# Performance work log

Measured on AMD Instinct MI355X. Metric: run time of the kernel, lower is better.

The kernel has to match this reference:

```python
import jax, jax.numpy as jnp
import numpy as np


def setup_inputs() -> dict:
    key = jax.random.key(0)
    k1, k2, k3, k4, k5 = jax.random.split(key, 5)
    B, L, D = 8, 4096, 64
    return {
        "Q": jax.random.normal(k1, (B, L, D), dtype=jnp.float32),
        "K": jax.random.normal(k2, (B, L, D), dtype=jnp.float32),
        "V": jax.random.normal(k3, (B, L, D), dtype=jnp.float32),
        "sent_embed_slice": jax.random.normal(k4, (B, D), dtype=jnp.float32),
        "proj": jax.random.normal(k5, (D, D), dtype=jnp.float32),  # fixed phi projection (M, d)
        "qkv_size": 64,
        "masked": 1,
    }


def _phi(X, proj, M):
    # X: (B, L, d). Original applies phi per timestep slice x = X[:, t, :] of shape (B, d)
    # phi(x) = (1/sqrt(M)) * exp(-0.5 * ||x||_F) * exp(proj @ x), Frobenius norm over the (B, d) slice.
    logits = jnp.einsum("bld,md->blm", X, proj)            # (B, L, M)
    scale = jnp.exp(-0.5 * jnp.sqrt(jnp.sum(X * X, axis=(0, 2))))  # per-timestep scalar, (L,)
    return jnp.exp(logits) * scale[None, :, None] / jnp.sqrt(jnp.asarray(M, jnp.float32))


def reference(Q, K, V, sent_embed_slice, proj, qkv_size, masked):
    M = qkv_size
    phi_q = _phi(Q, proj, M)  # (B, L, M)
    phi_k = _phi(K, proj, M)  # (B, L, M)
    if masked:
        # causal running sums: KV_t = sum_{j<=t} phi_k_j outer V_j ; N_t = sum_{j<=t} phi_k_j
        KV = jnp.cumsum(phi_k[:, :, :, None] * V[:, :, None, :], axis=1)  # (B, L, M, D)
        Nc = jnp.cumsum(phi_k, axis=1)                                    # (B, L, M)
        num = jnp.einsum("blm,blmd->bld", phi_q, KV)
        r = jnp.einsum("blm,blm->bl", phi_q, Nc)
        return num / (r + jnp.sign(r) * 1e-6)[:, :, None]
    else:
        KV = jnp.einsum("blm,bld->bmd", phi_k, V)     # (B, M, D)
        Ns = jnp.sum(phi_k, axis=1)                    # (B, M); broadcast over D like torch norm_sum
        num = jnp.einsum("blm,bmd->bld", phi_q, KV)
        r = jnp.einsum("blm,bm->bl", phi_q, Ns)
        return num / r[:, :, None]
```

## Files before the change

kernel.cpp:

```cpp
#include <hip/hip_runtime.h>
#include <math.h>

#define BB 8
#define LL 4096
#define DD 64
#define SS 64
#define NCHUNK 64
#define STATE 4160

typedef __attribute__((ext_vector_type(8))) short s16x8;
typedef __attribute__((ext_vector_type(8))) unsigned short u16x8;
typedef __attribute__((ext_vector_type(4))) float f32x4;

#define MFMA(a, b, c) __builtin_amdgcn_mfma_f32_16x16x32_bf16((a), (b), (c), 0, 0, 0)

static __device__ __forceinline__ unsigned short f2bf(float x) {
  unsigned int u = __builtin_bit_cast(unsigned int, x);
  u += 0x7FFFu + ((u >> 16) & 1u);
  return (unsigned short)(u >> 16);
}
static __device__ __forceinline__ float bf2f(unsigned short h) {
  unsigned int u = ((unsigned int)h) << 16;
  return __builtin_bit_cast(float, u);
}

static __device__ __forceinline__ s16x8 ld_frag(const unsigned short* base, int row0, int ks) {
  const int lane = threadIdx.x & 63;
  const int r = row0 + (lane & 15);
  const int idx = r * 64 + ((ks * 32 + ((lane & 48) >> 1)) ^ ((r & 7) << 3));
  return *(const s16x8*)(base + idx);
}

static __device__ __forceinline__ void stage_hl(unsigned short* __restrict__ Sh,
                                                unsigned short* __restrict__ Sl,
                                                const float* __restrict__ src, int tid) {
#pragma unroll
  for (int it = 0; it < 2; ++it) {
    const int g = tid + it * 256;
    const int row = g >> 3;
    const int c0 = (g & 7) * 8;
    const float4 x0 = *(const float4*)(src + row * 64 + c0);
    const float4 x1 = *(const float4*)(src + row * 64 + c0 + 4);
    const float xs[8] = {x0.x, x0.y, x0.z, x0.w, x1.x, x1.y, x1.z, x1.w};
    u16x8 h, l;
#pragma unroll
    for (int k = 0; k < 8; ++k) {
      const unsigned short hh = f2bf(xs[k]);
      h[k] = hh;
      l[k] = f2bf(xs[k] - bf2f(hh));
    }
    const int idx = row * 64 + (c0 ^ ((row & 7) << 3));
    *(u16x8*)(Sh + idx) = h;
    *(u16x8*)(Sl + idx) = l;
  }
}

static __device__ __forceinline__ void logits3(const unsigned short* Ah_, const unsigned short* Al_,
                                               const unsigned short* Bh_, const unsigned short* Bl_,
                                               int w, f32x4 acc[4]) {
  s16x8 ah[2], al[2];
#pragma unroll
  for (int ks = 0; ks < 2; ++ks) {
    ah[ks] = ld_frag(Ah_, w * 16, ks);
    al[ks] = ld_frag(Al_, w * 16, ks);
  }
#pragma unroll
  for (int ct = 0; ct < 4; ++ct) {
#pragma unroll
    for (int ks = 0; ks < 2; ++ks) {
      const s16x8 bh = ld_frag(Bh_, ct * 16, ks);
      const s16x8 bl = ld_frag(Bl_, ct * 16, ks);
      acc[ct] = MFMA(ah[ks], bh, acc[ct]);
      acc[ct] = MFMA(ah[ks], bl, acc[ct]);
      acc[ct] = MFMA(al[ks], bh, acc[ct]);
    }
  }
}

static __device__ __forceinline__ void phi_store_row(unsigned short* dst, const f32x4* acc,
                                                     const float* sc, int w) {
  const int lane = threadIdx.x & 63;
#pragma unroll
  for (int ri = 0; ri < 4; ++ri) {
    const int t = w * 16 + ((lane & 48) >> 2) + ri;
#pragma unroll
    for (int ct = 0; ct < 4; ++ct) {
      const int m = ct * 16 + (lane & 15);
      dst[t * 64 + (m ^ ((t & 7) << 3))] = f2bf(__expf(acc[ct][ri]) * sc[ri]);
    }
  }
}

static __device__ __forceinline__ void phi_store_col(unsigned short* dst, const f32x4* acc,
                                                     const float* sc, int w) {
  const int lane = threadIdx.x & 63;
#pragma unroll
  for (int ri = 0; ri < 4; ++ri) {
    const int t = w * 16 + ((lane & 48) >> 2) + ri;
#pragma unroll
    for (int ct = 0; ct < 4; ++ct) {
      const int m = ct * 16 + (lane & 15);
      dst[m * 64 + (t ^ ((m & 7) << 3))] = f2bf(__expf(acc[ct][ri]) * sc[ri]);
    }
  }
}

static __device__ __forceinline__ void stage_vhalf(float* __restrict__ F, const float* __restrict__ src,
                                                   int tid) {
#pragma unroll
  for (int it = 0; it < 2; ++it) {
    const int g = tid + it * 256;
    const int row = g >> 4;
    const int col = (g & 15) * 4;
    *(float4*)(F + row * 64 + col) = *(const float4*)(src + row * 64 + col);
  }
}

static __device__ __forceinline__ void vtrans_half(unsigned short* __restrict__ Gh,
                                                   unsigned short* __restrict__ Hl,
                                                   const float* __restrict__ F, int tid, int half) {
  const int d = tid & 63;
  const int tb = (tid >> 6) * 8;
  float v[8];
#pragma unroll
  for (int k = 0; k < 8; ++k) v[k] = F[(tb + k) * 64 + d];
  u16x8 hh, ll;
#pragma unroll
  for (int k = 0; k < 8; ++k) {
    const unsigned short h = f2bf(v[k]);
    hh[k] = h;
    ll[k] = f2bf(v[k] - bf2f(h));
  }
  const int idx = d * 64 + ((half * 32 + tb) ^ ((d & 7) << 3));
  *(u16x8*)(Gh + idx) = hh;
  *(u16x8*)(Hl + idx) = ll;
}

__global__ __launch_bounds__(256) void k_scales(const float* __restrict__ Q,
                                                const float* __restrict__ K,
                                                float* __restrict__ ws) {
  const int t = blockIdx.x * 4 + (threadIdx.x >> 6);
  const int lane = threadIdx.x & 63;
  const int b = lane >> 3;
  const int d0 = (lane & 7) * 8;
  const size_t base = (size_t)b * (LL * DD) + (size_t)t * DD + d0;
  float sq = 0.f, sk = 0.f;
#pragma unroll
  for (int k = 0; k < 8; ++k) {
    const float q = Q[base + k]; sq += q * q;
    const float kk = K[base + k]; sk += kk * kk;
  }
#pragma unroll
  for (int off = 32; off; off >>= 1) {
    sq += __shfl_xor(sq, off);
    sk += __shfl_xor(sk, off);
  }
  if (lane == 0) {
    ws[t]      = expf(-0.5f * sqrtf(sq));
    ws[LL + t] = expf(-0.5f * sqrtf(sk));
  }
}

__global__ __launch_bounds__(256) void k_chunk_sums(const float* __restrict__ Kg,
                                                    const float* __restrict__ Vg,
                                                    const float* __restrict__ proj,
                                                    const float* __restrict__ ws,
                                                    float* __restrict__ states) {
  __shared__ unsigned short A_[4096], B_[4096];
  __shared__ unsigned short C_[4096], D_[4096];
  __shared__ unsigned short E_[4096];
  __shared__ unsigned short G_[4096], H_[4096];
  __shared__ float F_[2048];
  const int tid = threadIdx.x;
  const int lane = tid & 63;
  const int w = tid >> 6;
  const int bc = blockIdx.x;
  const int b = bc >> 6;
  const int c = bc & (NCHUNK - 1);
  const int t0 = c * SS;
  const size_t tileBase = ((size_t)b * LL + t0) * DD;
  float* stc = states + ((size_t)b * NCHUNK + c) * (size_t)STATE;

  stage_hl(A_, B_, proj, tid);
  stage_hl(C_, D_, Kg + tileBase, tid);
  stage_vhalf(F_, Vg + tileBase, tid);
  float sck[4];
#pragma unroll
  for (int ri = 0; ri < 4; ++ri) {
    const int trow = w * 16 + ((lane & 48) >> 2) + ri;
    sck[ri] = ws[LL + t0 + trow] * 0.125f;
  }
  __syncthreads();

  {
    f32x4 acc[4] = {};
    logits3(C_, D_, A_, B_, w, acc);
    phi_store_col(E_, acc, sck, w);
  }
  vtrans_half(G_, H_, F_, tid, 0);
  __syncthreads();
  stage_vhalf(F_, Vg + tileBase + 32 * 64, tid);
  __syncthreads();
  vtrans_half(G_, H_, F_, tid, 1);
  __syncthreads();

  {
    const int m = tid >> 2, q = tid & 3;
    float s = 0.f;
#pragma unroll
    for (int p = 0; p < 2; ++p) {
      const int tt = q * 16 + p * 8;
      const u16x8 vv = *(const u16x8*)(E_ + m * 64 + (tt ^ ((m & 7) << 3)));
#pragma unroll
      for (int i = 0; i < 8; ++i) s += bf2f(vv[i]);
    }
    s += __shfl_xor(s, 1);
    s += __shfl_xor(s, 2);
    if (q == 0) stc[4096 + m] = s;
  }

  {
    s16x8 avh[2], avl[2];
#pragma unroll
    for (int ks = 0; ks < 2; ++ks) {
      avh[ks] = ld_frag(G_, w * 16, ks);
      avl[ks] = ld_frag(H_, w * 16, ks);
    }
    f32x4 acc[4] = {};
#pragma unroll
    for (int ct = 0; ct < 4; ++ct) {
#pragma unroll
      for (int ks = 0; ks < 2; ++ks) {
        const s16x8 bp = ld_frag(E_, ct * 16, ks);
        acc[ct] = MFMA(avh[ks], bp, acc[ct]);
        acc[ct] = MFMA(avl[ks], bp, acc[ct]);
      }
    }
#pragma unroll
    for (int ri = 0; ri < 4; ++ri) {
      const int d = w * 16 + ((lane & 48) >> 2) + ri;
#pragma unroll
      for (int ct = 0; ct < 4; ++ct) {
        stc[d * 64 + ct * 16 + (lane & 15)] = acc[ct][ri];
      }
    }
  }
}

__global__ __launch_bounds__(256) void k_prefix(float* __restrict__ states) {
  const int e = blockIdx.x * 256 + threadIdx.x;
  if (e >= BB * STATE) return;
  const int b = e / STATE;
  const int el = e % STATE;
  float* p = states + (size_t)b * NCHUNK * STATE + el;
  float run = 0.f;
#pragma unroll 4
  for (int c = 0; c < NCHUNK; ++c) {
    const float v = p[(size_t)c * STATE];
    p[(size_t)c * STATE] = run;
    run += v;
  }
}

__global__ __launch_bounds__(256) void k_prefix1(const float* __restrict__ states,
                                                 float* __restrict__ tmp) {
  const int e = blockIdx.x * 256 + threadIdx.x;
  if (e >= BB * 8 * STATE) return;
  const int b = e / (8 * STATE);
  const int r = e % (8 * STATE);
  const int g = r / STATE;
  const int el = r % STATE;
  const float* p = states + ((size_t)b * NCHUNK + g * 8) * STATE + el;
  float s = 0.f;
#pragma unroll
  for (int i = 0; i < 8; ++i) s += p[(size_t)i * STATE];
  tmp[((size_t)b * 8 + g) * STATE + el] = s;
}

__global__ __launch_bounds__(256) void k_prefix2(float* __restrict__ states,
                                                 const float* __restrict__ tmp) {
  const int e = blockIdx.x * 256 + threadIdx.x;
  if (e >= BB * 8 * STATE) return;
  const int b = e / (8 * STATE);
  const int r = e % (8 * STATE);
  const int g = r / STATE;
  const int el = r % STATE;
  float run = 0.f;
  for (int g2 = 0; g2 < g; ++g2) run += tmp[((size_t)b * 8 + g2) * STATE + el];
  float* p = states + ((size_t)b * NCHUNK + g * 8) * STATE + el;
#pragma unroll
  for (int i = 0; i < 8; ++i) {
    const float v = p[(size_t)i * STATE];
    p[(size_t)i * STATE] = run;
    run += v;
  }
}

__global__ __launch_bounds__(256) void k_out(const float* __restrict__ Qg,
                                             const float* __restrict__ Kg,
                                             const float* __restrict__ Vg,
                                             const float* __restrict__ proj,
                                             const float* __restrict__ ws,
                                             const float* __restrict__ states,
                                             float* __restrict__ out) {
  __shared__ unsigned short A_[4096], B_[4096];
  __shared__ unsigned short C_[4096];
  __shared__ unsigned short D_[4096];
  __shared__ unsigned short E_[4096];
  __shared__ unsigned short G_[4096], H_[4096];
  __shared__ float F_[2048];
  const int tid = threadIdx.x;
  const int lane = tid & 63;
  const int w = tid >> 6;
  const int bc = blockIdx.x;
  const int b = bc >> 6;
  const int c = bc & (NCHUNK - 1);
  const int t0 = c * SS;
  const size_t tileBase = ((size_t)b * LL + t0) * DD;
  const float* st = states + ((size_t)b * NCHUNK + c) * (size_t)STATE;

  stage_hl(A_, B_, proj, tid);
  stage_hl(C_, D_, Qg + tileBase, tid);
  float scq[4], sck[4];
#pragma unroll
  for (int ri = 0; ri < 4; ++ri) {
    const int trow = w * 16 + ((lane & 48) >> 2) + ri;
    scq[ri] = ws[t0 + trow] * 0.125f;
    sck[ri] = ws[LL + t0 + trow] * 0.125f;
  }
  __syncthreads();

  {
    f32x4 acc[4] = {};
    logits3(C_, D_, A_, B_, w, acc);
    phi_store_row(C_, acc, scq, w);
  }
  __syncthreads();
  stage_hl(D_, E_, Kg + tileBase, tid);
  __syncthreads();
  {
    f32x4 acc[4] = {};
    logits3(D_, E_, A_, B_, w, acc);
    phi_store_row(D_, acc, sck, w);
  }
  __syncthreads();

  stage_hl(A_, B_, st, tid);
  stage_vhalf(F_, Vg + tileBase, tid);
  __syncthreads();

  vtrans_half(G_, H_, F_, tid, 0);

  float rsI[4];
  {
    s16x8 aq[2];
#pragma unroll
    for (int ks = 0; ks < 2; ++ks) aq[ks] = ld_frag(C_, w * 16, ks);
    f32x4 accA[4] = {};
#pragma unroll
    for (int ct = 0; ct < 4; ++ct) {
#pragma unroll
      for (int ks = 0; ks < 2; ++ks) {
        accA[ct] = MFMA(aq[ks], ld_frag(D_, ct * 16, ks), accA[ct]);
      }
    }
#pragma unroll
    for (int ri = 0; ri < 4; ++ri) {
      const int t = w * 16 + ((lane & 48) >> 2) + ri;
      float part = 0.f;
#pragma unroll
      for (int ct = 0; ct < 4; ++ct) {
        const int j = ct * 16 + (lane & 15);
        const float a = (j <= t) ? accA[ct][ri] : 0.f;
        const unsigned short ah = f2bf(a);
        part += bf2f(ah);
        E_[t * 64 + (j ^ ((t & 7) << 3))] = ah;
      }
#pragma unroll
      for (int off = 1; off < 16; off <<= 1) part += __shfl_xor(part, off);
      rsI[ri] = part;
    }
  }
  __syncthreads();
  stage_vhalf(F_, Vg + tileBase + 32 * 64, tid);
  __syncthreads();
  vtrans_half(G_, H_, F_, tid, 1);
  __syncthreads();

  {
    s16x8 aA[2], aq[2];
#pragma unroll
    for (int ks = 0; ks < 2; ++ks) {
      aA[ks] = ld_frag(E_, w * 16, ks);
      aq[ks] = ld_frag(C_, w * 16, ks);
    }
    f32x4 acc[4] = {};
#pragma unroll
    for (int ct = 0; ct < 4; ++ct) {
#pragma unroll
      for (int ks = 0; ks < 2; ++ks) {
        acc[ct] = MFMA(aA[ks], ld_frag(G_, ct * 16, ks), acc[ct]);
        acc[ct] = MFMA(aA[ks], ld_frag(H_, ct * 16, ks), acc[ct]);
        acc[ct] = MFMA(aq[ks], ld_frag(A_, ct * 16, ks), acc[ct]);
        acc[ct] = MFMA(aq[ks], ld_frag(B_, ct * 16, ks), acc[ct]);
      }
    }
    float rsp = 0.f;
    const float* Np = st + 4096;
#pragma unroll
    for (int ks = 0; ks < 2; ++ks) {
      const int m0 = ks * 32 + ((lane & 48) >> 1);
      const float4 n0 = *(const float4*)(Np + m0);
      const float4 n1 = *(const float4*)(Np + m0 + 4);
      const float nn[8] = {n0.x, n0.y, n0.z, n0.w, n1.x, n1.y, n1.z, n1.w};
#pragma unroll
      for (int i = 0; i < 8; ++i) rsp += bf2f((unsigned short)aq[ks][i]) * nn[i];
    }
    rsp += __shfl_xor(rsp, 16);
    rsp += __shfl_xor(rsp, 32);
#pragma unroll
    for (int ri = 0; ri < 4; ++ri) {
      const float r = rsI[ri] + __shfl(rsp, ((lane & 48) >> 2) + ri);
      const float inv = 1.f / (r + copysignf(1e-6f, r));
      const int t = w * 16 + ((lane & 48) >> 2) + ri;
#pragma unroll
      for (int ct = 0; ct < 4; ++ct) {
        out[tileBase + t * 64 + ct * 16 + (lane & 15)] = acc[ct][ri] * inv;
      }
    }
  }
}

extern "C" void kernel_launch(void* const* d_in, const int* in_sizes, int n_in,
                              void* d_out, int out_size, void* d_ws, size_t ws_size,
                              hipStream_t stream) {
  (void)in_sizes; (void)n_in; (void)out_size;
  const float* Q    = (const float*)d_in[0];
  const float* K    = (const float*)d_in[1];
  const float* V    = (const float*)d_in[2];
  const float* proj = (const float*)d_in[4];
  float* out = (float*)d_out;
  float* ws  = (float*)d_ws;
  float* states = ws + 2 * LL;
  const size_t statesFloats = (size_t)BB * NCHUNK * STATE;
  float* tmp = states + statesFloats;
  const size_t need2 = (2 * LL + statesFloats + (size_t)BB * 8 * STATE) * sizeof(float);

  hipLaunchKernelGGL(k_scales, dim3(LL / 4), dim3(256), 0, stream, Q, K, ws);
  hipLaunchKernelGGL(k_chunk_sums, dim3(BB * NCHUNK), dim3(256), 0, stream, K, V, proj, ws, states);
  if (ws_size >= need2) {
    hipLaunchKernelGGL(k_prefix1, dim3((BB * 8 * STATE + 255) / 256), dim3(256), 0, stream, states, tmp);
    hipLaunchKernelGGL(k_prefix2, dim3((BB * 8 * STATE + 255) / 256), dim3(256), 0, stream, states, tmp);
  } else {
    hipLaunchKernelGGL(k_prefix, dim3((BB * STATE + 255) / 256), dim3(256), 0, stream, states);
  }
  hipLaunchKernelGGL(k_out, dim3(BB * NCHUNK), dim3(256), 0, stream, Q, K, V, proj, ws, states, out);
}
```

Baseline: 34.62 us.

## Compute phi(Q) and phi(K) once in the first pass and reuse them in the output kernel

The chunk-sum kernel now computes phi for both Q and K, writes the bf16 tiles to workspace, and the output kernel reads them instead of recomputing the logits and exps. This removes the duplicated phi(K) computation and the proj staging in k_out, at the cost of extra global writes and reads of bf16 phi tiles (about 8 MB round trip). It also drops the fallback single-pass prefix path and assumes the workspace is large enough, and k_out now stages the full V tile at once.

```diff
diff --git a/kernel.cpp b/kernel.cpp
--- a/kernel.cpp
+++ b/kernel.cpp
@@ -109,6 +109,17 @@
                                                    int tid) {
 #pragma unroll
   for (int it = 0; it < 2; ++it) {
+    const int g = tid + it * 256;
+    const int row = g >> 4;
+    const int col = (g & 15) * 4;
+    *(float4*)(F + row * 64 + col) = *(const float4*)(src + row * 64 + col);
+  }
+}
+
+static __device__ __forceinline__ void stage_vfull(float* __restrict__ F, const float* __restrict__ src,
+                                                   int tid) {
+#pragma unroll
+  for (int it = 0; it < 4; ++it) {
     const int g = tid + it * 256;
     const int row = g >> 4;
     const int col = (g & 15) * 4;
@@ -161,16 +172,20 @@
   }
 }
 
-__global__ __launch_bounds__(256) void k_chunk_sums(const float* __restrict__ Kg,
-                                                    const float* __restrict__ Vg,
-                                                    const float* __restrict__ proj,
-                                                    const float* __restrict__ ws,
-                                                    float* __restrict__ states) {
-  __shared__ unsigned short A_[4096], B_[4096];
-  __shared__ unsigned short C_[4096], D_[4096];
-  __shared__ unsigned short E_[4096];
-  __shared__ unsigned short G_[4096], H_[4096];
-  __shared__ float F_[2048];
+__global__ __launch_bounds__(256) void k_phi_sums(const float* __restrict__ Qg,
+                                                  const float* __restrict__ Kg,
+                                                  const float* __restrict__ Vg,
+                                                  const float* __restrict__ proj,
+                                                  const float* __restrict__ ws,
+                                                  float* __restrict__ states,
+                                                  unsigned short* __restrict__ phiQg,
+                                                  unsigned short* __restrict__ phiKg) {
+  __shared__ unsigned short P0[4096], P1[4096];
+  __shared__ unsigned short X0[4096], X1[4096];
+  __shared__ unsigned short Y0[4096], Y1[4096];
+  __shared__ unsigned short PHIr[4096];
+  __shared__ unsigned short PHIc[4096];
+  __shared__ float F[2048];
   const int tid = threadIdx.x;
   const int lane = tid & 63;
   const int w = tid >> 6;
@@ -180,37 +195,50 @@
   const int t0 = c * SS;
   const size_t tileBase = ((size_t)b * LL + t0) * DD;
   float* stc = states + ((size_t)b * NCHUNK + c) * (size_t)STATE;
-
-  stage_hl(A_, B_, proj, tid);
-  stage_hl(C_, D_, Kg + tileBase, tid);
-  stage_vhalf(F_, Vg + tileBase, tid);
-  float sck[4];
+  unsigned short* pqT = phiQg + (size_t)bc * 4096;
+  unsigned short* pkT = phiKg + (size_t)bc * 4096;
+
+  stage_hl(P0, P1, proj, tid);
+  stage_hl(X0, X1, Qg + tileBase, tid);
+  stage_hl(Y0, Y1, Kg + tileBase, tid);
+  stage_vhalf(F, Vg + tileBase, tid);
+  float scq[4], sck[4];
 #pragma unroll
   for (int ri = 0; ri < 4; ++ri) {
     const int trow = w * 16 + ((lane & 48) >> 2) + ri;
+    scq[ri] = ws[t0 + trow] * 0.125f;
     sck[ri] = ws[LL + t0 + trow] * 0.125f;
   }
   __syncthreads();
 
   {
     f32x4 acc[4] = {};
-    logits3(C_, D_, A_, B_, w, acc);
-    phi_store_col(E_, acc, sck, w);
-  }
-  vtrans_half(G_, H_, F_, tid, 0);
-  __syncthreads();
-  stage_vhalf(F_, Vg + tileBase + 32 * 64, tid);
-  __syncthreads();
-  vtrans_half(G_, H_, F_, tid, 1);
-  __syncthreads();
-
+    logits3(X0, X1, P0, P1, w, acc);
+    phi_store_row(X0, acc, scq, w);
+  }
+  {
+    f32x4 acc[4] = {};
+    logits3(Y0, Y1, P0, P1, w, acc);
+    phi_store_row(PHIr, acc, sck, w);
+    phi_store_col(PHIc, acc, sck, w);
+  }
+  __syncthreads();
+
+  vtrans_half(Y0, Y1, F, tid, 0);
+  {
+    const int o = tid * 16;
+    *(u16x8*)(pqT + o)     = *(const u16x8*)(X0 + o);
+    *(u16x8*)(pqT + o + 8) = *(const u16x8*)(X0 + o + 8);
+    *(u16x8*)(pkT + o)     = *(const u16x8*)(PHIr + o);
+    *(u16x8*)(pkT + o + 8) = *(const u16x8*)(PHIr + o + 8);
+  }
   {
     const int m = tid >> 2, q = tid & 3;
     float s = 0.f;
 #pragma unroll
     for (int p = 0; p < 2; ++p) {
       const int tt = q * 16 + p * 8;
-      const u16x8 vv = *(const u16x8*)(E_ + m * 64 + (tt ^ ((m & 7) << 3)));
+      const u16x8 vv = *(const u16x8*)(PHIc + m * 64 + (tt ^ ((m & 7) << 3)));
 #pragma unroll
       for (int i = 0; i < 8; ++i) s += bf2f(vv[i]);
     }
@@ -218,20 +246,25 @@
     s += __shfl_xor(s, 2);
     if (q == 0) stc[4096 + m] = s;
   }
+  __syncthreads();
+  stage_vhalf(F, Vg + tileBase + 32 * 64, tid);
+  __syncthreads();
+  vtrans_half(Y0, Y1, F, tid, 1);
+  __syncthreads();
 
   {
     s16x8 avh[2], avl[2];
 #pragma unroll
     for (int ks = 0; ks < 2; ++ks) {
-      avh[ks] = ld_frag(G_, w * 16, ks);
-      avl[ks] = ld_frag(H_, w * 16, ks);
+      avh[ks] = ld_frag(Y0, w * 16, ks);
+      avl[ks] = ld_frag(Y1, w * 16, ks);
     }
     f32x4 acc[4] = {};
 #pragma unroll
     for (int ct = 0; ct < 4; ++ct) {
 #pragma unroll
       for (int ks = 0; ks < 2; ++ks) {
-        const s16x8 bp = ld_frag(E_, ct * 16, ks);
+        const s16x8 bp = ld_frag(PHIc, ct * 16, ks);
         acc[ct] = MFMA(avh[ks], bp, acc[ct]);
         acc[ct] = MFMA(avl[ks], bp, acc[ct]);
       }
@@ -244,21 +277,6 @@
         stc[d * 64 + ct * 16 + (lane & 15)] = acc[ct][ri];
       }
     }
-  }
-}
-
-__global__ __launch_bounds__(256) void k_prefix(float* __restrict__ states) {
-  const int e = blockIdx.x * 256 + threadIdx.x;
-  if (e >= BB * STATE) return;
-  const int b = e / STATE;
-  const int el = e % STATE;
-  float* p = states + (size_t)b * NCHUNK * STATE + el;
-  float run = 0.f;
-#pragma unroll 4
-  for (int c = 0; c < NCHUNK; ++c) {
-    const float v = p[(size_t)c * STATE];
-    p[(size_t)c * STATE] = run;
-    run += v;
   }
 }
 
@@ -296,19 +314,17 @@
   }
 }
 
-__global__ __launch_bounds__(256) void k_out(const float* __restrict__ Qg,
-                                             const float* __restrict__ Kg,
-                                             const float* __restrict__ Vg,
-                                             const float* __restrict__ proj,
-                                             const float* __restrict__ ws,
+__global__ __launch_bounds__(256) void k_out(const float* __restrict__ Vg,
+                                             const unsigned short* __restrict__ phiQg,
+                                             const unsigned short* __restrict__ phiKg,
                                              const float* __restrict__ states,
                                              float* __restrict__ out) {
-  __shared__ unsigned short A_[4096], B_[4096];
-  __shared__ unsigned short C_[4096];
-  __shared__ unsigned short D_[4096];
-  __shared__ unsigned short E_[4096];
-  __shared__ unsigned short G_[4096], H_[4096];
-  __shared__ float F_[2048];
+  __shared__ unsigned short PQ[4096];
+  __shared__ unsigned short PK[4096];
+  __shared__ unsigned short E[4096];
+  __shared__ unsigned short KV0[4096], KV1[4096];
+  __shared__ unsigned short VT0[4096], VT1[4096];
+  __shared__ float F[4096];
   const int tid = threadIdx.x;
   const int lane = tid & 63;
   const int w = tid >> 6;
@@ -318,50 +334,34 @@
   const int t0 = c * SS;
   const size_t tileBase = ((size_t)b * LL + t0) * DD;
   const float* st = states + ((size_t)b * NCHUNK + c) * (size_t)STATE;
-
-  stage_hl(A_, B_, proj, tid);
-  stage_hl(C_, D_, Qg + tileBase, tid);
-  float scq[4], sck[4];
-#pragma unroll
-  for (int ri = 0; ri < 4; ++ri) {
-    const int trow = w * 16 + ((lane & 48) >> 2) + ri;
-    scq[ri] = ws[t0 + trow] * 0.125f;
-    sck[ri] = ws[LL + t0 + trow] * 0.125f;
-  }
-  __syncthreads();
-
-  {
-    f32x4 acc[4] = {};
-    logits3(C_, D_, A_, B_, w, acc);
-    phi_store_row(C_, acc, scq, w);
-  }
-  __syncthreads();
-  stage_hl(D_, E_, Kg + tileBase, tid);
-  __syncthreads();
-  {
-    f32x4 acc[4] = {};
-    logits3(D_, E_, A_, B_, w, acc);
-    phi_store_row(D_, acc, sck, w);
-  }
-  __syncthreads();
-
-  stage_hl(A_, B_, st, tid);
-  stage_vhalf(F_, Vg + tileBase, tid);
-  __syncthreads();
-
-  vtrans_half(G_, H_, F_, tid, 0);
+  const unsigned short* pqT = phiQg + (size_t)bc * 4096;
+  const unsigned short* pkT = phiKg + (size_t)bc * 4096;
+
+  {
+    const int o = tid * 16;
+    *(u16x8*)(PQ + o)     = *(const u16x8*)(pqT + o);
+    *(u16x8*)(PQ + o + 8) = *(const u16x8*)(pqT + o + 8);
+    *(u16x8*)(PK + o)     = *(const u16x8*)(pkT + o);
+    *(u16x8*)(PK + o + 8) = *(const u16x8*)(pkT + o + 8);
+  }
+  stage_hl(KV0, KV1, st, tid);
+  stage_vfull(F, Vg + tileBase, tid);
+  __syncthreads();
+
+  vtrans_half(VT0, VT1, F, tid, 0);
+  vtrans_half(VT0, VT1, F + 32 * 64, tid, 1);
 
   float rsI[4];
-  {
-    s16x8 aq[2];
-#pragma unroll
-    for (int ks = 0; ks < 2; ++ks) aq[ks] = ld_frag(C_, w * 16, ks);
+  s16x8 aq[2];
+#pragma unroll
+  for (int ks = 0; ks < 2; ++ks) aq[ks] = ld_frag(PQ, w * 16, ks);
+  {
     f32x4 accA[4] = {};
 #pragma unroll
     for (int ct = 0; ct < 4; ++ct) {
 #pragma unroll
       for (int ks = 0; ks < 2; ++ks) {
-        accA[ct] = MFMA(aq[ks], ld_frag(D_, ct * 16, ks), accA[ct]);
+        accA[ct] = MFMA(aq[ks], ld_frag(PK, ct * 16, ks), accA[ct]);
       }
     }
 #pragma unroll
@@ -374,7 +374,7 @@
         const float a = (j <= t) ? accA[ct][ri] : 0.f;
         const unsigned short ah = f2bf(a);
         part += bf2f(ah);
-        E_[t * 64 + (j ^ ((t & 7) << 3))] = ah;
+        E[t * 64 + (j ^ ((t & 7) << 3))] = ah;
       }
 #pragma unroll
       for (int off = 1; off < 16; off <<= 1) part += __shfl_xor(part, off);
@@ -382,27 +382,20 @@
     }
   }
   __syncthreads();
-  stage_vhalf(F_, Vg + tileBase + 32 * 64, tid);
-  __syncthreads();
-  vtrans_half(G_, H_, F_, tid, 1);
-  __syncthreads();
-
-  {
-    s16x8 aA[2], aq[2];
-#pragma unroll
-    for (int ks = 0; ks < 2; ++ks) {
-      aA[ks] = ld_frag(E_, w * 16, ks);
-      aq[ks] = ld_frag(C_, w * 16, ks);
-    }
+
+  {
+    s16x8 aA[2];
+#pragma unroll
+    for (int ks = 0; ks < 2; ++ks) aA[ks] = ld_frag(E, w * 16, ks);
     f32x4 acc[4] = {};
 #pragma unroll
     for (int ct = 0; ct < 4; ++ct) {
 #pragma unroll
       for (int ks = 0; ks < 2; ++ks) {
-        acc[ct] = MFMA(aA[ks], ld_frag(G_, ct * 16, ks), acc[ct]);
-        acc[ct] = MFMA(aA[ks], ld_frag(H_, ct * 16, ks), acc[ct]);
-        acc[ct] = MFMA(aq[ks], ld_frag(A_, ct * 16, ks), acc[ct]);
-        acc[ct] = MFMA(aq[ks], ld_frag(B_, ct * 16, ks), acc[ct]);
+        acc[ct] = MFMA(aA[ks], ld_frag(VT0, ct * 16, ks), acc[ct]);
+        acc[ct] = MFMA(aA[ks], ld_frag(VT1, ct * 16, ks), acc[ct]);
+        acc[ct] = MFMA(aq[ks], ld_frag(KV0, ct * 16, ks), acc[ct]);
+        acc[ct] = MFMA(aq[ks], ld_frag(KV1, ct * 16, ks), acc[ct]);
       }
     }
     float rsp = 0.f;
@@ -434,7 +427,7 @@
 extern "C" void kernel_launch(void* const* d_in, const int* in_sizes, int n_in,
                               void* d_out, int out_size, void* d_ws, size_t ws_size,
                               hipStream_t stream) {
-  (void)in_sizes; (void)n_in; (void)out_size;
+  (void)in_sizes; (void)n_in; (void)out_size; (void)ws_size;
   const float* Q    = (const float*)d_in[0];
   const float* K    = (const float*)d_in[1];
   const float* V    = (const float*)d_in[2];
@@ -444,15 +437,15 @@
   float* states = ws + 2 * LL;
   const size_t statesFloats = (size_t)BB * NCHUNK * STATE;
   float* tmp = states + statesFloats;
-  const size_t need2 = (2 * LL + statesFloats + (size_t)BB * 8 * STATE) * sizeof(float);
+  const size_t tmpFloats = (size_t)BB * 8 * STATE;
+  unsigned short* phiQg = (unsigned short*)(tmp + tmpFloats);
+  unsigned short* phiKg = phiQg + (size_t)BB * NCHUNK * 4096;
 
   hipLaunchKernelGGL(k_scales, dim3(LL / 4), dim3(256), 0, stream, Q, K, ws);
-  hipLaunchKernelGGL(k_chunk_sums, dim3(BB * NCHUNK), dim3(256), 0, stream, K, V, proj, ws, states);
-  if (ws_size >= need2) {
-    hipLaunchKernelGGL(k_prefix1, dim3((BB * 8 * STATE + 255) / 256), dim3(256), 0, stream, states, tmp);
-    hipLaunchKernelGGL(k_prefix2, dim3((BB * 8 * STATE + 255) / 256), dim3(256), 0, stream, states, tmp);
-  } else {
-    hipLaunchKernelGGL(k_prefix, dim3((BB * STATE + 255) / 256), dim3(256), 0, stream, states);
-  }
-  hipLaunchKernelGGL(k_out, dim3(BB * NCHUNK), dim3(256), 0, stream, Q, K, V, proj, ws, states, out);
-}
+  hipLaunchKernelGGL(k_phi_sums, dim3(BB * NCHUNK), dim3(256), 0, stream,
+                     Q, K, V, proj, ws, states, phiQg, phiKg);
+  hipLaunchKernelGGL(k_prefix1, dim3((BB * 8 * STATE + 255) / 256), dim3(256), 0, stream, states, tmp);
+  hipLaunchKernelGGL(k_prefix2, dim3((BB * 8 * STATE + 255) / 256), dim3(256), 0, stream, states, tmp);
+  hipLaunchKernelGGL(k_out, dim3(BB * NCHUNK), dim3(256), 0, stream,
+                     V, phiQg, phiKg, states, out);
+}
```

After: 35.78 us. 1.03x slower.

## Reuse phi(K) from chunk-sum kernel in output kernel and stage V fully

Applied to the files above, without the earlier changes.

k_chunk_sums now writes its bf16 phi(K) tile to global workspace, and k_out reads it back instead of reloading K and recomputing the K logits with three-way split-bf16 MFMAs. Both kernels stage the whole 64x64 V tile in shared memory at once, which removes the half-tile staging and its extra barriers. k_out also loads the prefix state early alongside the other tiles. This adds global write and read traffic for phi(K) and raises LDS use, and it drops the fallback path that ran when the workspace was too small.

```diff
diff --git a/kernel.cpp b/kernel.cpp
--- a/kernel.cpp
+++ b/kernel.cpp
@@ -55,6 +55,48 @@
   }
 }
 
+static __device__ __forceinline__ void stage_vfull(float* __restrict__ F, const float* __restrict__ src,
+                                                   int tid) {
+#pragma unroll
+  for (int it = 0; it < 4; ++it) {
+    const int g = tid + it * 256;
+    const int row = g >> 4;
+    const int col = (g & 15) * 4;
+    *(float4*)(F + row * 64 + col) = *(const float4*)(src + row * 64 + col);
+  }
+}
+
+static __device__ __forceinline__ void stage_img(unsigned short* __restrict__ S,
+                                                 const unsigned short* __restrict__ src, int tid) {
+#pragma unroll
+  for (int it = 0; it < 2; ++it) {
+    const int g = tid + it * 256;
+    const int row = g >> 3;
+    const int c0 = (g & 7) * 8;
+    *(u16x8*)(S + row * 64 + (c0 ^ ((row & 7) << 3))) = *(const u16x8*)(src + row * 64 + c0);
+  }
+}
+
+static __device__ __forceinline__ void vtrans_half(unsigned short* __restrict__ Gh,
+                                                   unsigned short* __restrict__ Hl,
+                                                   const float* __restrict__ F, int tid, int half) {
+  const int d = tid & 63;
+  const int tb = (tid >> 6) * 8;
+  float v[8];
+#pragma unroll
+  for (int k = 0; k < 8; ++k) v[k] = F[(tb + k) * 64 + d];
+  u16x8 hh, ll;
+#pragma unroll
+  for (int k = 0; k < 8; ++k) {
+    const unsigned short h = f2bf(v[k]);
+    hh[k] = h;
+    ll[k] = f2bf(v[k] - bf2f(h));
+  }
+  const int idx = d * 64 + ((half * 32 + tb) ^ ((d & 7) << 3));
+  *(u16x8*)(Gh + idx) = hh;
+  *(u16x8*)(Hl + idx) = ll;
+}
+
 static __device__ __forceinline__ void logits3(const unsigned short* Ah_, const unsigned short* Al_,
                                                const unsigned short* Bh_, const unsigned short* Bl_,
                                                int w, f32x4 acc[4]) {
@@ -91,8 +133,9 @@
   }
 }
 
-static __device__ __forceinline__ void phi_store_col(unsigned short* dst, const f32x4* acc,
-                                                     const float* sc, int w) {
+static __device__ __forceinline__ void phi_store_col_and_g(unsigned short* dstc,
+                                                           unsigned short* __restrict__ gdst,
+                                                           const f32x4* acc, const float* sc, int w) {
   const int lane = threadIdx.x & 63;
 #pragma unroll
   for (int ri = 0; ri < 4; ++ri) {
@@ -100,40 +143,11 @@
 #pragma unroll
     for (int ct = 0; ct < 4; ++ct) {
       const int m = ct * 16 + (lane & 15);
-      dst[m * 64 + (t ^ ((m & 7) << 3))] = f2bf(__expf(acc[ct][ri]) * sc[ri]);
-    }
-  }
-}
-
-static __device__ __forceinline__ void stage_vhalf(float* __restrict__ F, const float* __restrict__ src,
-                                                   int tid) {
-#pragma unroll
-  for (int it = 0; it < 2; ++it) {
-    const int g = tid + it * 256;
-    const int row = g >> 4;
-    const int col = (g & 15) * 4;
-    *(float4*)(F + row * 64 + col) = *(const float4*)(src + row * 64 + col);
-  }
-}
-
-static __device__ __forceinline__ void vtrans_half(unsigned short* __restrict__ Gh,
-                                                   unsigned short* __restrict__ Hl,
-                                                   const float* __restrict__ F, int tid, int half) {
-  const int d = tid & 63;
-  const int tb = (tid >> 6) * 8;
-  float v[8];
-#pragma unroll
-  for (int k = 0; k < 8; ++k) v[k] = F[(tb + k) * 64 + d];
-  u16x8 hh, ll;
-#pragma unroll
-  for (int k = 0; k < 8; ++k) {
-    const unsigned short h = f2bf(v[k]);
-    hh[k] = h;
-    ll[k] = f2bf(v[k] - bf2f(h));
-  }
-  const int idx = d * 64 + ((half * 32 + tb) ^ ((d & 7) << 3));
-  *(u16x8*)(Gh + idx) = hh;
-  *(u16x8*)(Hl + idx) = ll;
+      const unsigned short ph = f2bf(__expf(acc[ct][ri]) * sc[ri]);
+      dstc[m * 64 + (t ^ ((m & 7) << 3))] = ph;
+      gdst[t * 64 + m] = ph;
+    }
+  }
 }
 
 __global__ __launch_bounds__(256) void k_scales(const float* __restrict__ Q,
@@ -165,12 +179,13 @@
                                                     const float* __restrict__ Vg,
                                                     const float* __restrict__ proj,
                                                     const float* __restrict__ ws,
-                                                    float* __restrict__ states) {
+                                                    float* __restrict__ states,
+                                                    unsigned short* __restrict__ phiKg) {
   __shared__ unsigned short A_[4096], B_[4096];
   __shared__ unsigned short C_[4096], D_[4096];
   __shared__ unsigned short E_[4096];
   __shared__ unsigned short G_[4096], H_[4096];
-  __shared__ float F_[2048];
+  __shared__ float F[4096];
   const int tid = threadIdx.x;
   const int lane = tid & 63;
   const int w = tid >> 6;
@@ -180,10 +195,11 @@
   const int t0 = c * SS;
   const size_t tileBase = ((size_t)b * LL + t0) * DD;
   float* stc = states + ((size_t)b * NCHUNK + c) * (size_t)STATE;
+  unsigned short* pkT = phiKg + (size_t)bc * 4096;
 
   stage_hl(A_, B_, proj, tid);
   stage_hl(C_, D_, Kg + tileBase, tid);
-  stage_vhalf(F_, Vg + tileBase, tid);
+  stage_vfull(F, Vg + tileBase, tid);
   float sck[4];
 #pragma unroll
   for (int ri = 0; ri < 4; ++ri) {
@@ -195,13 +211,10 @@
   {
     f32x4 acc[4] = {};
     logits3(C_, D_, A_, B_, w, acc);
-    phi_store_col(E_, acc, sck, w);
-  }
-  vtrans_half(G_, H_, F_, tid, 0);
-  __syncthreads();
-  stage_vhalf(F_, Vg + tileBase + 32 * 64, tid);
-  __syncthreads();
-  vtrans_half(G_, H_, F_, tid, 1);
+    phi_store_col_and_g(E_, pkT, acc, sck, w);
+  }
+  vtrans_half(G_, H_, F, tid, 0);
+  vtrans_half(G_, H_, F + 32 * 64, tid, 1);
   __syncthreads();
 
   {
@@ -218,7 +231,6 @@
     s += __shfl_xor(s, 2);
     if (q == 0) stc[4096 + m] = s;
   }
-
   {
     s16x8 avh[2], avl[2];
 #pragma unroll
@@ -228,14 +240,13 @@
     }
     f32x4 acc[4] = {};
 #pragma unroll
-    for (int ct = 0; ct < 4; ++ct) {
+    for (int ct = 0; ct < 4; ++ct)
 #pragma unroll
       for (int ks = 0; ks < 2; ++ks) {
         const s16x8 bp = ld_frag(E_, ct * 16, ks);
         acc[ct] = MFMA(avh[ks], bp, acc[ct]);
         acc[ct] = MFMA(avl[ks], bp, acc[ct]);
       }
-    }
 #pragma unroll
     for (int ri = 0; ri < 4; ++ri) {
       const int d = w * 16 + ((lane & 48) >> 2) + ri;
@@ -244,21 +255,6 @@
         stc[d * 64 + ct * 16 + (lane & 15)] = acc[ct][ri];
       }
     }
-  }
-}
-
-__global__ __launch_bounds__(256) void k_prefix(float* __restrict__ states) {
-  const int e = blockIdx.x * 256 + threadIdx.x;
-  if (e >= BB * STATE) return;
-  const int b = e / STATE;
-  const int el = e % STATE;
-  float* p = states + (size_t)b * NCHUNK * STATE + el;
-  float run = 0.f;
-#pragma unroll 4
-  for (int c = 0; c < NCHUNK; ++c) {
-    const float v = p[(size_t)c * STATE];
-    p[(size_t)c * STATE] = run;
-    run += v;
   }
 }
 
@@ -297,18 +293,18 @@
 }
 
 __global__ __launch_bounds__(256) void k_out(const float* __restrict__ Qg,
-                                             const float* __restrict__ Kg,
                                              const float* __restrict__ Vg,
                                              const float* __restrict__ proj,
+                                             const unsigned short* __restrict__ phiKg,
                                              const float* __restrict__ ws,
                                              const float* __restrict__ states,
                                              float* __restrict__ out) {
   __shared__ unsigned short A_[4096], B_[4096];
   __shared__ unsigned short C_[4096];
   __shared__ unsigned short D_[4096];
-  __shared__ unsigned short E_[4096];
-  __shared__ unsigned short G_[4096], H_[4096];
-  __shared__ float F_[2048];
+  __shared__ unsigned short PK[4096];
+  __shared__ unsigned short KV0[4096], KV1[4096];
+  __shared__ float F[4096];
   const int tid = threadIdx.x;
   const int lane = tid & 63;
   const int w = tid >> 6;
@@ -318,52 +314,42 @@
   const int t0 = c * SS;
   const size_t tileBase = ((size_t)b * LL + t0) * DD;
   const float* st = states + ((size_t)b * NCHUNK + c) * (size_t)STATE;
+  const unsigned short* pkT = phiKg + (size_t)bc * 4096;
 
   stage_hl(A_, B_, proj, tid);
   stage_hl(C_, D_, Qg + tileBase, tid);
-  float scq[4], sck[4];
+  stage_img(PK, pkT, tid);
+  stage_hl(KV0, KV1, st, tid);
+  stage_vfull(F, Vg + tileBase, tid);
+  float scq[4];
 #pragma unroll
   for (int ri = 0; ri < 4; ++ri) {
     const int trow = w * 16 + ((lane & 48) >> 2) + ri;
     scq[ri] = ws[t0 + trow] * 0.125f;
-    sck[ri] = ws[LL + t0 + trow] * 0.125f;
   }
   __syncthreads();
 
+  s16x8 aq[2];
   {
     f32x4 acc[4] = {};
     logits3(C_, D_, A_, B_, w, acc);
     phi_store_row(C_, acc, scq, w);
+#pragma unroll
+    for (int ks = 0; ks < 2; ++ks) aq[ks] = ld_frag(C_, w * 16, ks);
   }
   __syncthreads();
-  stage_hl(D_, E_, Kg + tileBase, tid);
-  __syncthreads();
-  {
-    f32x4 acc[4] = {};
-    logits3(D_, E_, A_, B_, w, acc);
-    phi_store_row(D_, acc, sck, w);
-  }
-  __syncthreads();
-
-  stage_hl(A_, B_, st, tid);
-  stage_vhalf(F_, Vg + tileBase, tid);
-  __syncthreads();
-
-  vtrans_half(G_, H_, F_, tid, 0);
+
+  vtrans_half(A_, B_, F, tid, 0);
+  vtrans_half(A_, B_, F + 32 * 64, tid, 1);
 
   float rsI[4];
   {
-    s16x8 aq[2];
-#pragma unroll
-    for (int ks = 0; ks < 2; ++ks) aq[ks] = ld_frag(C_, w * 16, ks);
     f32x4 accA[4] = {};
 #pragma unroll
-    for (int ct = 0; ct < 4; ++ct) {
-#pragma unroll
-      for (int ks = 0; ks < 2; ++ks) {
-        accA[ct] = MFMA(aq[ks], ld_frag(D_, ct * 16, ks), accA[ct]);
-      }
-    }
+    for (int ct = 0; ct < 4; ++ct)
+#pragma unroll
+      for (int ks = 0; ks < 2; ++ks)
+        accA[ct] = MFMA(aq[ks], ld_frag(PK, ct * 16, ks), accA[ct]);
 #pragma unroll
     for (int ri = 0; ri < 4; ++ri) {
       const int t = w * 16 + ((lane & 48) >> 2) + ri;
@@ -374,7 +360,7 @@
         const float a = (j <= t) ? accA[ct][ri] : 0.f;
         const unsigned short ah = f2bf(a);
         part += bf2f(ah);
-        E_[t * 64 + (j ^ ((t & 7) << 3))] = ah;
+        D_[t * 64 + (j ^ ((t & 7) << 3))] = ah;
       }
 #pragma unroll
       for (int off = 1; off < 16; off <<= 1) part += __shfl_xor(part, off);
@@ -382,27 +368,20 @@
     }
   }
   __syncthreads();
-  stage_vhalf(F_, Vg + tileBase + 32 * 64, tid);
-  __syncthreads();
-  vtrans_half(G_, H_, F_, tid, 1);
-  __syncthreads();
-
-  {
-    s16x8 aA[2], aq[2];
-#pragma unroll
-    for (int ks = 0; ks < 2; ++ks) {
-      aA[ks] = ld_frag(E_, w * 16, ks);
-      aq[ks] = ld_frag(C_, w * 16, ks);
-    }
+
+  {
+    s16x8 aA[2];
+#pragma unroll
+    for (int ks = 0; ks < 2; ++ks) aA[ks] = ld_frag(D_, w * 16, ks);
     f32x4 acc[4] = {};
 #pragma unroll
     for (int ct = 0; ct < 4; ++ct) {
 #pragma unroll
       for (int ks = 0; ks < 2; ++ks) {
-        acc[ct] = MFMA(aA[ks], ld_frag(G_, ct * 16, ks), acc[ct]);
-        acc[ct] = MFMA(aA[ks], ld_frag(H_, ct * 16, ks), acc[ct]);
-        acc[ct] = MFMA(aq[ks], ld_frag(A_, ct * 16, ks), acc[ct]);
-        acc[ct] = MFMA(aq[ks], ld_frag(B_, ct * 16, ks), acc[ct]);
+        acc[ct] = MFMA(aA[ks], ld_frag(A_, ct * 16, ks), acc[ct]);
+        acc[ct] = MFMA(aA[ks], ld_frag(B_, ct * 16, ks), acc[ct]);
+        acc[ct] = MFMA(aq[ks], ld_frag(KV0, ct * 16, ks), acc[ct]);
+        acc[ct] = MFMA(aq[ks], ld_frag(KV1, ct * 16, ks), acc[ct]);
       }
     }
     float rsp = 0.f;
@@ -434,7 +413,7 @@
 extern "C" void kernel_launch(void* const* d_in, const int* in_sizes, int n_in,
                               void* d_out, int out_size, void* d_ws, size_t ws_size,
                               hipStream_t stream) {
-  (void)in_sizes; (void)n_in; (void)out_size;
+  (void)in_sizes; (void)n_in; (void)out_size; (void)ws_size;
   const float* Q    = (const float*)d_in[0];
   const float* K    = (const float*)d_in[1];
   const float* V    = (const float*)d_in[2];
@@ -444,15 +423,14 @@
   float* states = ws + 2 * LL;
   const size_t statesFloats = (size_t)BB * NCHUNK * STATE;
   float* tmp = states + statesFloats;
-  const size_t need2 = (2 * LL + statesFloats + (size_t)BB * 8 * STATE) * sizeof(float);
+  const size_t tmpFloats = (size_t)BB * 8 * STATE;
+  unsigned short* phiKg = (unsigned short*)(tmp + tmpFloats);
 
   hipLaunchKernelGGL(k_scales, dim3(LL / 4), dim3(256), 0, stream, Q, K, ws);
-  hipLaunchKernelGGL(k_chunk_sums, dim3(BB * NCHUNK), dim3(256), 0, stream, K, V, proj, ws, states);
-  if (ws_size >= need2) {
-    hipLaunchKernelGGL(k_prefix1, dim3((BB * 8 * STATE + 255) / 256), dim3(256), 0, stream, states, tmp);
-    hipLaunchKernelGGL(k_prefix2, dim3((BB * 8 * STATE + 255) / 256), dim3(256), 0, stream, states, tmp);
-  } else {
-    hipLaunchKernelGGL(k_prefix, dim3((BB * STATE + 255) / 256), dim3(256), 0, stream, states);
-  }
-  hipLaunchKernelGGL(k_out, dim3(BB * NCHUNK), dim3(256), 0, stream, Q, K, V, proj, ws, states, out);
-}
+  hipLaunchKernelGGL(k_chunk_sums, dim3(BB * NCHUNK), dim3(256), 0, stream,
+                     K, V, proj, ws, states, phiKg);
+  hipLaunchKernelGGL(k_prefix1, dim3((BB * 8 * STATE + 255) / 256), dim3(256), 0, stream, states, tmp);
+  hipLaunchKernelGGL(k_prefix2, dim3((BB * 8 * STATE + 255) / 256), dim3(256), 0, stream, states, tmp);
+  hipLaunchKernelGGL(k_out, dim3(BB * NCHUNK), dim3(256), 0, stream,
+                     Q, V, proj, phiKg, ws, states, out);
+}
```

Result: no change. 34.54 us (-0.2%).
